# Performance work log

Measured on AMD Instinct MI355X. Metric: run time of the kernel, lower is better.

The kernel has to match this reference:

```python
import jax, jax.numpy as jnp
import numpy as np

INPUT_SIZE = 1024
HIDDEN_SIZE = 1024
N_LAYERS = 2
OUTPUT_SIZE = 4096
BATCH = 4096


def setup_inputs() -> dict:
    key = jax.random.key(0)
    ks = jax.random.split(key, 12)
    s = 1.0 / np.sqrt(HIDDEN_SIZE)
    u = lambda k, shp: jax.random.uniform(k, shp, jnp.float32, -s, s)
    return {
        "input": jax.random.normal(ks[0], (1, BATCH, INPUT_SIZE), jnp.float32),
        "hidden": jax.random.normal(ks[1], (N_LAYERS, BATCH, HIDDEN_SIZE), jnp.float32),
        # nn.RNN layer 0 params
        "W_ih0": u(ks[2], (HIDDEN_SIZE, INPUT_SIZE)),
        "W_hh0": u(ks[3], (HIDDEN_SIZE, HIDDEN_SIZE)),
        "b_ih0": u(ks[4], (HIDDEN_SIZE,)),
        "b_hh0": u(ks[5], (HIDDEN_SIZE,)),
        # nn.RNN layer 1 params (input is layer-0 hidden)
        "W_ih1": u(ks[6], (HIDDEN_SIZE, HIDDEN_SIZE)),
        "W_hh1": u(ks[7], (HIDDEN_SIZE, HIDDEN_SIZE)),
        "b_ih1": u(ks[8], (HIDDEN_SIZE,)),
        "b_hh1": u(ks[9], (HIDDEN_SIZE,)),
        # i2o Linear(input_size + hidden_size, output_size)
        "W_out": u(ks[10], (OUTPUT_SIZE, INPUT_SIZE + HIDDEN_SIZE)),
        "b_out": u(ks[11], (OUTPUT_SIZE,)),
    }


def reference(input, hidden, W_ih0, W_hh0, b_ih0, b_hh0,
              W_ih1, W_hh1, b_ih1, b_hh1, W_out, b_out):
    x = input[0]  # [B, input_size] (seq_len == 1)
    # nn.RNN single step, tanh nonlinearity, 2 layers
    h0 = jnp.tanh(x @ W_ih0.T + b_ih0 + hidden[0] @ W_hh0.T + b_hh0)   # [B, H]
    h1 = jnp.tanh(h0 @ W_ih1.T + b_ih1 + hidden[1] @ W_hh1.T + b_hh1)  # [B, H]
    new_hidden = jnp.stack([h0, h1], axis=0)  # [n_layers, B, H]
    # combined = cat(input[0], hidden[0]) where hidden is the NEW hidden
    combined = jnp.concatenate([x, h0], axis=1)  # [B, input+hidden]
    logits = combined @ W_out.T + b_out          # [B, output_size]
    out = jax.nn.log_softmax(logits, axis=1)
    return (out, new_hidden)
```

## Files before the change

### kernel.cpp

```cpp
#include <hip/hip_runtime.h>
#include <math.h>


typedef __attribute__((ext_vector_type(8))) short bf16x8;
typedef __attribute__((ext_vector_type(4))) float f32x4;

__device__ __forceinline__ unsigned short f2b_rne(float f) {
    unsigned int x = __float_as_uint(f);
    x += 0x7FFF + ((x >> 16) & 1);
    return (unsigned short)(x >> 16);
}

__device__ __forceinline__ void gload_lds16(const void* g, void* l) {
    __builtin_amdgcn_global_load_lds(
        (const __attribute__((address_space(1))) void*)g,
        (__attribute__((address_space(3))) void*)l,
        16, 0, 0);
}

struct CvtSeg { const float* src; unsigned short* dst; unsigned n8; };
struct CvtArgs { CvtSeg seg[8]; };

__global__ __launch_bounds__(256) void f2b_multi(CvtArgs a)
{
    unsigned i = blockIdx.x * 256u + threadIdx.x;
#pragma unroll
    for (int s = 0; s < 8; ++s) {
        if (i < a.seg[s].n8) {
            const float4* src = (const float4*)a.seg[s].src;
            float4 u = src[2 * (size_t)i];
            float4 v = src[2 * (size_t)i + 1];
            unsigned short t[8] = {
                f2b_rne(u.x), f2b_rne(u.y), f2b_rne(u.z), f2b_rne(u.w),
                f2b_rne(v.x), f2b_rne(v.y), f2b_rne(v.z), f2b_rne(v.w)};
            *(uint4*)(a.seg[s].dst + 8 * (size_t)i) = *(const uint4*)t;
            return;
        }
        i -= a.seg[s].n8;
    }
}

struct GemmP {
    const unsigned short *Aa, *Ab; int lda;
    const unsigned short *Wa, *Wb; int ldw;
    const float *ba, *bb;
    float* C; int ldc;
    unsigned short* Cb; int ldcb;
    int nx, nb, do_tanh;
};

template<int BM, int BN>
__device__ __forceinline__ void gemm2p_body(
    const GemmP& p, int bid0, unsigned short* As, unsigned short* Ws, int tid)
{
    constexpr int FM = BM / 32;
    constexpr int FN = BN / 32;
    int bid = (bid0 & 7) * (p.nb >> 3) + (bid0 >> 3);
    const int row0 = (bid / p.nx) * BM;
    const int col0 = (bid % p.nx) * BN;

    const int wid = tid >> 6, lane = tid & 63;
    const int wr = wid >> 1, wc = wid & 1;
    const int fr = lane & 15, fk = lane >> 4;

    f32x4 acc[FM][FN] = {};

    for (int h = 0; h < 2; ++h) {
        const unsigned short* A = h ? p.Ab : p.Aa;
        const unsigned short* W = h ? p.Wb : p.Wa;
        for (int k0 = 0; k0 < 1024; k0 += 64) {
#pragma unroll
            for (int i = 0; i < BM / 32; ++i) {
                int c = i * 256 + wid * 64 + lane;
                int r = c >> 3, cc = c & 7;
                int gk = k0 + (((cc ^ r) & 7) << 3);
                gload_lds16(A + (size_t)(row0 + r) * p.lda + gk,
                            As + (i * 256 + wid * 64) * 8);
            }
#pragma unroll
            for (int i = 0; i < BN / 32; ++i) {
                int c = i * 256 + wid * 64 + lane;
                int r = c >> 3, cc = c & 7;
                int gk = k0 + (((cc ^ r) & 7) << 3);
                gload_lds16(W + (size_t)(col0 + r) * p.ldw + gk,
                            Ws + (i * 256 + wid * 64) * 8);
            }
            __syncthreads();

            bf16x8 af[FM][2], wf[FN][2];
#pragma unroll
            for (int m = 0; m < FM; ++m) {
                int r = wr * (BM / 2) + m * 16 + fr;
                int cc = fk ^ (r & 7);
                af[m][0] = *(const bf16x8*)&As[r * 64 + cc * 8];
                af[m][1] = *(const bf16x8*)&As[r * 64 + (cc ^ 4) * 8];
            }
#pragma unroll
            for (int n = 0; n < FN; ++n) {
                int r = wc * (BN / 2) + n * 16 + fr;
                int cc = fk ^ (r & 7);
                wf[n][0] = *(const bf16x8*)&Ws[r * 64 + cc * 8];
                wf[n][1] = *(const bf16x8*)&Ws[r * 64 + (cc ^ 4) * 8];
            }
#pragma unroll
            for (int m = 0; m < FM; ++m)
#pragma unroll
                for (int n = 0; n < FN; ++n) {
                    acc[m][n] = __builtin_amdgcn_mfma_f32_16x16x32_bf16(
                        af[m][0], wf[n][0], acc[m][n], 0, 0, 0);
                    acc[m][n] = __builtin_amdgcn_mfma_f32_16x16x32_bf16(
                        af[m][1], wf[n][1], acc[m][n], 0, 0, 0);
                }
            __syncthreads();
        }
    }

    const bool dot = p.do_tanh != 0;
#pragma unroll
    for (int n = 0; n < FN; ++n) {
        const int col = col0 + wc * (BN / 2) + n * 16 + fr;
        float b = p.ba[col];
        if (p.bb) b += p.bb[col];
#pragma unroll
        for (int m = 0; m < FM; ++m) {
#pragma unroll
            for (int j = 0; j < 4; ++j) {
                const int r = row0 + wr * (BM / 2) + m * 16 + fk * 4 + j;
                float v = acc[m][n][j] + b;
                if (dot) v = tanhf(v);
                p.C[(size_t)r * p.ldc + col] = v;
                if (p.Cb) p.Cb[(size_t)r * p.ldcb + col] = f2b_rne(v);
            }
        }
    }
}

__global__ __launch_bounds__(256) void gemm1_k(GemmP p)
{
    __shared__ __align__(16) unsigned short As[128 * 64];
    __shared__ __align__(16) unsigned short Ws[64 * 64];
    gemm2p_body<128, 64>(p, blockIdx.x, As, Ws, threadIdx.x);
}

__device__ __forceinline__ void logsoftmax_row_b16(
    const unsigned short* __restrict__ lb, float* __restrict__ op, int tid)
{
    const int lane = tid & 63;
    const int wv = tid >> 6;
    __shared__ float redm[4];
    __shared__ float reds[4];

    uint4 r[2];
    r[0] = *(const uint4*)&lb[tid * 8];
    r[1] = *(const uint4*)&lb[2048 + tid * 8];
    float v[16];
#pragma unroll
    for (int h = 0; h < 2; ++h)
#pragma unroll
        for (int j = 0; j < 4; ++j) {
            unsigned u = ((const unsigned*)&r[h])[j];
            v[h * 8 + 2 * j]     = __uint_as_float(u << 16);
            v[h * 8 + 2 * j + 1] = __uint_as_float(u & 0xFFFF0000u);
        }

    float m = v[0];
#pragma unroll
    for (int i = 1; i < 16; ++i) m = fmaxf(m, v[i]);
#pragma unroll
    for (int off = 32; off; off >>= 1) m = fmaxf(m, __shfl_xor(m, off));
    if (lane == 0) redm[wv] = m;
    __syncthreads();
    m = fmaxf(fmaxf(redm[0], redm[1]), fmaxf(redm[2], redm[3]));

    float s = 0.f;
#pragma unroll
    for (int i = 0; i < 16; ++i) s += expf(v[i] - m);
#pragma unroll
    for (int off = 32; off; off >>= 1) s += __shfl_xor(s, off);
    if (lane == 0) reds[wv] = s;
    __syncthreads();
    s = reds[0] + reds[1] + reds[2] + reds[3];

    const float lse = m + logf(s);
#pragma unroll
    for (int h = 0; h < 2; ++h) {
        float4 o0, o1;
        o0.x = v[h*8+0]-lse; o0.y = v[h*8+1]-lse; o0.z = v[h*8+2]-lse; o0.w = v[h*8+3]-lse;
        o1.x = v[h*8+4]-lse; o1.y = v[h*8+5]-lse; o1.z = v[h*8+6]-lse; o1.w = v[h*8+7]-lse;
        *(float4*)&op[h * 2048 + tid * 8]     = o0;
        *(float4*)&op[h * 2048 + tid * 8 + 4] = o1;
    }
}

__global__ __launch_bounds__(256) void g2sm_k(
    GemmP p, float* __restrict__ out, const unsigned short* __restrict__ lb16)
{
    if (blockIdx.x < 512) {
        __shared__ __align__(16) unsigned short As[128 * 64];
        __shared__ __align__(16) unsigned short Ws[64 * 64];
        gemm2p_body<128, 64>(p, blockIdx.x, As, Ws, threadIdx.x);
    } else {
        const int row = blockIdx.x - 512;
        logsoftmax_row_b16(lb16 + (size_t)row * 4096,
                           out + (size_t)row * 4096, threadIdx.x);
    }
}


__device__ __forceinline__ void stage_half8(
    const unsigned short* __restrict__ src, int ld, int base_rc, int tau, int h,
    unsigned short* lds, int wid, int lane, bool isA)
{
    unsigned short* dst = lds + (tau & 1) * 16384 + h * 8192 + wid * 1024;
    const int k0 = (tau & 15) << 6;
#pragma unroll
    for (int i = 0; i < 2; ++i) {
        int c = wid * 128 + i * 64 + lane;
        int ir = c >> 3, cc = c & 7;
        int grow = isA ? (base_rc + h * 64 + (ir & 63) + ((ir >> 6) << 7))
                       : (base_rc + h * 32 + (ir & 31) + ((ir >> 5) << 6));
        int gk = k0 + (((cc ^ ir) & 7) << 3);
        gload_lds16(src + (size_t)grow * ld + gk, dst + i * 512);
    }
}

__global__ __launch_bounds__(512, 2) void gemm8p(
    const unsigned short* __restrict__ Aa, const unsigned short* __restrict__ Ab,
    const unsigned short* __restrict__ Wa, const unsigned short* __restrict__ Wb,
    int lda, int ldw, const float* __restrict__ bias,
    unsigned short* __restrict__ Cb16, int ldc, int nx)
{
    constexpr int NT = 32;
    __shared__ __align__(16) unsigned short smem[65536];
    unsigned short* As = smem;
    unsigned short* Bs = smem + 32768;

    int bid = blockIdx.x;
    bid = (bid & 7) * 32 + (bid >> 3);
    const int row0 = (bid / nx) * 256;
    const int col0 = (bid % nx) * 256;

    const int tid = threadIdx.x;
    const int wid = tid >> 6, lane = tid & 63;
    const int wr = wid >> 2, wc = wid & 3;
    const int fr = lane & 15, fk = lane >> 4;
    const int ch0 = fk ^ (fr & 7);
    const int ch1 = ch0 ^ 4;

#define STA8(tau, h) stage_half8(((tau) < 16 ? Aa : Ab), lda, row0, (tau), (h), As, wid, lane, true)
#define STB8(tau, h) stage_half8(((tau) < 16 ? Wa : Wb), ldw, col0, (tau), (h), Bs, wid, lane, false)

#define LDAF(QM) { const unsigned short* Ap_ = Abase + (QM) * 8192;           \
    _Pragma("unroll") for (int mf = 0; mf < 4; ++mf) {                        \
        int ia = wr * 64 + mf * 16 + fr;                                      \
        af[mf][0] = *(const bf16x8*)&Ap_[ia * 64 + ch0 * 8];                  \
        af[mf][1] = *(const bf16x8*)&Ap_[ia * 64 + ch1 * 8]; } }

#define LDWF(QN, WF) { const unsigned short* Bp_ = Bbase + (QN) * 8192;       \
    _Pragma("unroll") for (int nf = 0; nf < 2; ++nf) {                        \
        int ib = wc * 32 + nf * 16 + fr;                                      \
        WF[nf][0] = *(const bf16x8*)&Bp_[ib * 64 + ch0 * 8];                  \
        WF[nf][1] = *(const bf16x8*)&Bp_[ib * 64 + ch1 * 8]; } }

#define MMQ(QM, QN, WF) {                                                     \
    __builtin_amdgcn_s_setprio(1);                                            \
    _Pragma("unroll") for (int mf = 0; mf < 4; ++mf)                          \
    _Pragma("unroll") for (int nf = 0; nf < 2; ++nf) {                        \
        acc[QM][QN][mf][nf] = __builtin_amdgcn_mfma_f32_16x16x32_bf16(        \
            af[mf][0], WF[nf][0], acc[QM][QN][mf][nf], 0, 0, 0);              \
        acc[QM][QN][mf][nf] = __builtin_amdgcn_mfma_f32_16x16x32_bf16(        \
            af[mf][1], WF[nf][1], acc[QM][QN][mf][nf], 0, 0, 0); }            \
    __builtin_amdgcn_s_setprio(0); }

    f32x4 acc[2][2][4][2] = {};
    bf16x8 af[4][2], wfA[2][2], wfB[2][2];

    STA8(0, 0); STB8(0, 0); STB8(0, 1); STA8(0, 1);

    for (int t = 0; t < NT; ++t) {
        const unsigned short* Abase = As + (t & 1) * 16384;
        const unsigned short* Bbase = Bs + (t & 1) * 16384;
        const bool more = (t + 1 < NT);

        asm volatile("s_waitcnt vmcnt(4)" ::: "memory");
        __builtin_amdgcn_s_barrier();
        LDAF(0); LDWF(0, wfA);
        if (more) STA8(t + 1, 0);
        MMQ(0, 0, wfA);

        if (more) { asm volatile("s_waitcnt vmcnt(4)" ::: "memory"); }
        else      { asm volatile("s_waitcnt vmcnt(2)" ::: "memory"); }
        __builtin_amdgcn_s_barrier();
        LDWF(1, wfB);
        if (more) STB8(t + 1, 0);
        MMQ(0, 1, wfB);

        if (more) { asm volatile("s_waitcnt vmcnt(4)" ::: "memory"); }
        else      { asm volatile("s_waitcnt vmcnt(0)" ::: "memory"); }
        __builtin_amdgcn_s_barrier();
        LDAF(1);
        if (more) STB8(t + 1, 1);
        MMQ(1, 1, wfB);

        if (more) STA8(t + 1, 1);
        MMQ(1, 0, wfA);
    }
#undef MMQ
#undef LDAF
#undef LDWF
#undef STA8
#undef STB8

    float bv[2][2];
#pragma unroll
    for (int qn = 0; qn < 2; ++qn)
#pragma unroll
        for (int nf = 0; nf < 2; ++nf)
            bv[qn][nf] = bias[col0 + wc * 64 + qn * 32 + nf * 16 + fr];

    float* Ct = (float*)smem;
    __syncthreads();
#pragma unroll
    for (int qm = 0; qm < 2; ++qm) {
        if (qm) __syncthreads();
#pragma unroll
        for (int qn = 0; qn < 2; ++qn)
#pragma unroll
            for (int nf = 0; nf < 2; ++nf) {
                const int col = wc * 64 + qn * 32 + nf * 16 + fr;
#pragma unroll
                for (int mf = 0; mf < 4; ++mf)
#pragma unroll
                    for (int j = 0; j < 4; ++j) {
                        int lr = wr * 64 + mf * 16 + fk * 4 + j;
                        int pc = col ^ (((lr >> 2) & 3) << 4);
                        Ct[lr * 256 + pc] = acc[qm][qn][mf][nf][j] + bv[qn][nf];
                    }
            }
        __syncthreads();
#pragma unroll
        for (int k = 0; k < 16; ++k) {
            int idx = k * 512 + tid;
            int lrow = idx >> 6, c4 = idx & 63;
            int pc4 = (c4 * 4) ^ (((lrow >> 2) & 3) << 4);
            int grow = row0 + qm * 64 + (lrow & 63) + ((lrow >> 6) << 7);
            float4 v = *(const float4*)&Ct[lrow * 256 + pc4];
            unsigned short o[4] = { f2b_rne(v.x), f2b_rne(v.y),
                                    f2b_rne(v.z), f2b_rne(v.w) };
            *(ushort4*)&Cb16[(size_t)grow * ldc + col0 + c4 * 4] =
                *(const ushort4*)o;
        }
    }
}

extern "C" void kernel_launch(void* const* d_in, const int* in_sizes, int n_in,
                              void* d_out, int out_size, void* d_ws, size_t ws_size,
                              hipStream_t stream)
{
    (void)in_sizes; (void)n_in; (void)out_size; (void)ws_size;

    const float* input  = (const float*)d_in[0];
    const float* hidden = (const float*)d_in[1];
    const float* b_ih0  = (const float*)d_in[4];
    const float* b_hh0  = (const float*)d_in[5];
    const float* b_ih1  = (const float*)d_in[8];
    const float* b_hh1  = (const float*)d_in[9];
    const float* b_out  = (const float*)d_in[11];

    float* out = (float*)d_out;
    float* h0  = out + (size_t)4096 * 4096;
    float* h1  = h0 + (size_t)4096 * 1024;

    unsigned short* xb    = (unsigned short*)d_ws;
    unsigned short* hidb  = xb    + (size_t)4096 * 1024;
    unsigned short* h0b   = hidb  + (size_t)2 * 4096 * 1024;
    unsigned short* Wih0b = h0b   + (size_t)4096 * 1024;
    unsigned short* Whh0b = Wih0b + (size_t)1024 * 1024;
    unsigned short* Wih1b = Whh0b + (size_t)1024 * 1024;
    unsigned short* Whh1b = Wih1b + (size_t)1024 * 1024;
    unsigned short* Woutb = Whh1b + (size_t)1024 * 1024;
    unsigned short* lb16  = Woutb + (size_t)4096 * 2048;
    unsigned short* hid0b = hidb;
    unsigned short* hid1b = hidb + (size_t)4096 * 1024;

    CvtArgs ca;
    ca.seg[0] = { input,                 xb,    524288u };
    ca.seg[1] = { hidden,                hidb, 1048576u };
    ca.seg[2] = { (const float*)d_in[2], Wih0b, 131072u };
    ca.seg[3] = { (const float*)d_in[3], Whh0b, 131072u };
    ca.seg[4] = { (const float*)d_in[6], Wih1b, 131072u };
    ca.seg[5] = { (const float*)d_in[7], Whh1b, 131072u };
    ca.seg[6] = { (const float*)d_in[10],Woutb, 1048576u };
    ca.seg[7] = { nullptr, nullptr, 0u };
    hipLaunchKernelGGL(f2b_multi, dim3(12288), dim3(256), 0, stream, ca);

    GemmP p1;
    p1.Aa = xb;    p1.Ab = hid0b; p1.lda = 1024;
    p1.Wa = Wih0b; p1.Wb = Whh0b; p1.ldw = 1024;
    p1.ba = b_ih0; p1.bb = b_hh0;
    p1.C = h0; p1.ldc = 1024; p1.Cb = h0b; p1.ldcb = 1024;
    p1.nx = 16; p1.nb = 512; p1.do_tanh = 1;
    hipLaunchKernelGGL(gemm1_k, dim3(512), dim3(256), 0, stream, p1);

    hipLaunchKernelGGL(gemm8p, dim3(256), dim3(512), 0, stream,
                       xb, h0b, Woutb, Woutb + 1024, 1024, 2048,
                       b_out, lb16, 4096, 16);

    GemmP p2;
    p2.Aa = h0b;   p2.Ab = hid1b; p2.lda = 1024;
    p2.Wa = Wih1b; p2.Wb = Whh1b; p2.ldw = 1024;
    p2.ba = b_ih1; p2.bb = b_hh1;
    p2.C = h1; p2.ldc = 1024; p2.Cb = nullptr; p2.ldcb = 0;
    p2.nx = 16; p2.nb = 512; p2.do_tanh = 1;
    hipLaunchKernelGGL(g2sm_k, dim3(4608), dim3(256), 0, stream, p2, out, lb16);
}
```

Measured before the change: 160.7 us.

## Double-buffer LDS tiles in two-part GEMM to overlap loads with MFMA

Flattens the two K-halves of the GEMM into a single 32-step loop and double-buffers the A and W LDS tiles. The next tile is prefetched via global_load_lds while MFMAs run on the current buffer, and a single waitcnt plus barrier ends each step. The goal is to hide global-load latency behind compute. In exchange, LDS use per block doubles to 48KB, which may lower occupancy.

```diff
diff --git a/kernel.cpp b/kernel.cpp
--- a/kernel.cpp
+++ b/kernel.cpp
@@ -55,6 +55,8 @@
 {
     constexpr int FM = BM / 32;
     constexpr int FN = BN / 32;
+    constexpr int ASZ = BM * 64;
+    constexpr int WSZ = BN * 64;
     int bid = (bid0 & 7) * (p.nb >> 3) + (bid0 >> 3);
     const int row0 = (bid / p.nx) * BM;
     const int col0 = (bid % p.nx) * BN;
@@ -65,55 +67,65 @@
 
     f32x4 acc[FM][FN] = {};
 
-    for (int h = 0; h < 2; ++h) {
-        const unsigned short* A = h ? p.Ab : p.Aa;
-        const unsigned short* W = h ? p.Wb : p.Wa;
-        for (int k0 = 0; k0 < 1024; k0 += 64) {
-#pragma unroll
-            for (int i = 0; i < BM / 32; ++i) {
-                int c = i * 256 + wid * 64 + lane;
-                int r = c >> 3, cc = c & 7;
-                int gk = k0 + (((cc ^ r) & 7) << 3);
-                gload_lds16(A + (size_t)(row0 + r) * p.lda + gk,
-                            As + (i * 256 + wid * 64) * 8);
+#define STAGE2P(kk, b) {                                                      \
+    const unsigned short* A_ = ((kk) < 16) ? p.Aa : p.Ab;                     \
+    const unsigned short* W_ = ((kk) < 16) ? p.Wa : p.Wb;                     \
+    const int k0_ = ((kk) & 15) << 6;                                         \
+    unsigned short* Ad_ = As + (b) * ASZ;                                     \
+    unsigned short* Wd_ = Ws + (b) * WSZ;                                     \
+    _Pragma("unroll") for (int i = 0; i < BM / 32; ++i) {                     \
+        int c = i * 256 + wid * 64 + lane;                                    \
+        int r = c >> 3, cc = c & 7;                                           \
+        int gk = k0_ + (((cc ^ r) & 7) << 3);                                 \
+        gload_lds16(A_ + (size_t)(row0 + r) * p.lda + gk,                     \
+                    Ad_ + (i * 256 + wid * 64) * 8);                          \
+    }                                                                         \
+    _Pragma("unroll") for (int i = 0; i < BN / 32; ++i) {                     \
+        int c = i * 256 + wid * 64 + lane;                                    \
+        int r = c >> 3, cc = c & 7;                                           \
+        int gk = k0_ + (((cc ^ r) & 7) << 3);                                 \
+        gload_lds16(W_ + (size_t)(col0 + r) * p.ldw + gk,                     \
+                    Wd_ + (i * 256 + wid * 64) * 8);                          \
+    } }
+
+    STAGE2P(0, 0);
+    asm volatile("s_waitcnt vmcnt(0)" ::: "memory");
+    __builtin_amdgcn_s_barrier();
+
+    for (int kk = 0; kk < 32; ++kk) {
+        const int cur = kk & 1;
+        if (kk + 1 < 32) STAGE2P(kk + 1, cur ^ 1);
+        const unsigned short* Ab_ = As + cur * ASZ;
+        const unsigned short* Wb_ = Ws + cur * WSZ;
+
+        bf16x8 af[FM][2], wf[FN][2];
+#pragma unroll
+        for (int m = 0; m < FM; ++m) {
+            int r = wr * (BM / 2) + m * 16 + fr;
+            int cc = fk ^ (r & 7);
+            af[m][0] = *(const bf16x8*)&Ab_[r * 64 + cc * 8];
+            af[m][1] = *(const bf16x8*)&Ab_[r * 64 + (cc ^ 4) * 8];
+        }
+#pragma unroll
+        for (int n = 0; n < FN; ++n) {
+            int r = wc * (BN / 2) + n * 16 + fr;
+            int cc = fk ^ (r & 7);
+            wf[n][0] = *(const bf16x8*)&Wb_[r * 64 + cc * 8];
+            wf[n][1] = *(const bf16x8*)&Wb_[r * 64 + (cc ^ 4) * 8];
+        }
+#pragma unroll
+        for (int m = 0; m < FM; ++m)
+#pragma unroll
+            for (int n = 0; n < FN; ++n) {
+                acc[m][n] = __builtin_amdgcn_mfma_f32_16x16x32_bf16(
+                    af[m][0], wf[n][0], acc[m][n], 0, 0, 0);
+                acc[m][n] = __builtin_amdgcn_mfma_f32_16x16x32_bf16(
+                    af[m][1], wf[n][1], acc[m][n], 0, 0, 0);
             }
-#pragma unroll
-            for (int i = 0; i < BN / 32; ++i) {
-                int c = i * 256 + wid * 64 + lane;
-                int r = c >> 3, cc = c & 7;
-                int gk = k0 + (((cc ^ r) & 7) << 3);
-                gload_lds16(W + (size_t)(col0 + r) * p.ldw + gk,
-                            Ws + (i * 256 + wid * 64) * 8);
-            }
-            __syncthreads();
-
-            bf16x8 af[FM][2], wf[FN][2];
-#pragma unroll
-            for (int m = 0; m < FM; ++m) {
-                int r = wr * (BM / 2) + m * 16 + fr;
-                int cc = fk ^ (r & 7);
-                af[m][0] = *(const bf16x8*)&As[r * 64 + cc * 8];
-                af[m][1] = *(const bf16x8*)&As[r * 64 + (cc ^ 4) * 8];
-            }
-#pragma unroll
-            for (int n = 0; n < FN; ++n) {
-                int r = wc * (BN / 2) + n * 16 + fr;
-                int cc = fk ^ (r & 7);
-                wf[n][0] = *(const bf16x8*)&Ws[r * 64 + cc * 8];
-                wf[n][1] = *(const bf16x8*)&Ws[r * 64 + (cc ^ 4) * 8];
-            }
-#pragma unroll
-            for (int m = 0; m < FM; ++m)
-#pragma unroll
-                for (int n = 0; n < FN; ++n) {
-                    acc[m][n] = __builtin_amdgcn_mfma_f32_16x16x32_bf16(
-                        af[m][0], wf[n][0], acc[m][n], 0, 0, 0);
-                    acc[m][n] = __builtin_amdgcn_mfma_f32_16x16x32_bf16(
-                        af[m][1], wf[n][1], acc[m][n], 0, 0, 0);
-                }
-            __syncthreads();
-        }
-    }
+        asm volatile("s_waitcnt vmcnt(0)" ::: "memory");
+        __builtin_amdgcn_s_barrier();
+    }
+#undef STAGE2P
 
     const bool dot = p.do_tanh != 0;
 #pragma unroll
@@ -137,8 +149,8 @@
 
 __global__ __launch_bounds__(256) void gemm1_k(GemmP p)
 {
-    __shared__ __align__(16) unsigned short As[128 * 64];
-    __shared__ __align__(16) unsigned short Ws[64 * 64];
+    __shared__ __align__(16) unsigned short As[2 * 128 * 64];
+    __shared__ __align__(16) unsigned short Ws[2 * 64 * 64];
     gemm2p_body<128, 64>(p, blockIdx.x, As, Ws, threadIdx.x);
 }
 
@@ -196,8 +208,8 @@
     GemmP p, float* __restrict__ out, const unsigned short* __restrict__ lb16)
 {
     if (blockIdx.x < 512) {
-        __shared__ __align__(16) unsigned short As[128 * 64];
-        __shared__ __align__(16) unsigned short Ws[64 * 64];
+        __shared__ __align__(16) unsigned short As[2 * 128 * 64];
+        __shared__ __align__(16) unsigned short Ws[2 * 64 * 64];
         gemm2p_body<128, 64>(p, blockIdx.x, As, Ws, threadIdx.x);
     } else {
         const int row = blockIdx.x - 512;
```

New measurement: 179.3 us. 1.12x slower.
